# Kernel optimization log

Hardware: AMD Instinct MI355X
Metric: run time of the kernel (lower is better)

## Reference

```python
import jax, jax.numpy as jnp
import numpy as np

N_NODES = 100000
N_EDGES = 1600000
N_GRAPHS = 64
IN_FEATS = 86  # 10 + |NodeTypes|(3) + |Devices|(5) + 2*2 + 2*32
GCN_H = 64
FC_H = 32
BN_EPS = 1e-5


def setup_inputs() -> dict:
    key = jax.random.key(0)
    ks = jax.random.split(key, 10)
    x = jax.random.normal(ks[0], (N_NODES, IN_FEATS), dtype=jnp.float32)
    edge_src = jax.random.randint(ks[1], (N_EDGES,), 0, N_NODES, dtype=jnp.int32)
    edge_dst = jax.random.randint(ks[2], (N_EDGES,), 0, N_NODES, dtype=jnp.int32)
    graph_ids = jnp.sort(jax.random.randint(ks[3], (N_NODES,), 0, N_GRAPHS, dtype=jnp.int32))
    bn_gamma = jnp.ones((IN_FEATS,), dtype=jnp.float32)
    bn_beta = jnp.zeros((IN_FEATS,), dtype=jnp.float32)
    W1 = jax.random.normal(ks[4], (IN_FEATS, GCN_H), dtype=jnp.float32) * 0.1
    b1 = jnp.zeros((GCN_H,), dtype=jnp.float32)
    W2 = jax.random.normal(ks[5], (GCN_H, GCN_H), dtype=jnp.float32) * 0.1
    b2 = jnp.zeros((GCN_H,), dtype=jnp.float32)
    fc1_w = jax.random.normal(ks[6], (GCN_H, FC_H), dtype=jnp.float32) * 0.1
    fc1_b = jnp.zeros((FC_H,), dtype=jnp.float32)
    fc2_w = jax.random.normal(ks[7], (FC_H, 1), dtype=jnp.float32) * 0.1
    fc2_b = jnp.zeros((1,), dtype=jnp.float32)
    return {"x": x, "edge_src": edge_src, "edge_dst": edge_dst,
            "graph_ids": graph_ids, "num_graphs": N_GRAPHS,
            "bn_gamma": bn_gamma, "bn_beta": bn_beta,
            "W1": W1, "b1": b1, "W2": W2, "b2": b2,
            "fc1_w": fc1_w, "fc1_b": fc1_b, "fc2_w": fc2_w, "fc2_b": fc2_b}


def _gcn_layer(h, edge_src, edge_dst, W, b):
    # DGL copy_src + mean reduce: each node's h is overwritten by the mean of
    # its in-neighbors' h; zero-in-degree nodes keep their old h (UDF reduce
    # is only applied to nodes with non-empty mailboxes).
    n = h.shape[0]
    msg_sum = jax.ops.segment_sum(h[edge_src], edge_dst, num_segments=n)  # [N, d]
    deg = jax.ops.segment_sum(jnp.ones_like(edge_dst, dtype=h.dtype), edge_dst, num_segments=n)
    agg = jnp.where(deg[:, None] > 0, msg_sum / jnp.maximum(deg, 1.0)[:, None], h)
    return jax.nn.relu(agg @ W + b)


def reference(x, edge_src, edge_dst, graph_ids, num_graphs,
              bn_gamma, bn_beta, W1, b1, W2, b2, fc1_w, fc1_b, fc2_w, fc2_b):
    # BatchNorm1d in training mode: batch stats, biased variance.
    mean = jnp.mean(x, axis=0)
    var = jnp.mean(jnp.square(x - mean), axis=0)
    h = (x - mean) * jax.lax.rsqrt(var + BN_EPS) * bn_gamma + bn_beta
    # Two GCN layers (mean message passing + linear + ReLU).
    h = _gcn_layer(h, edge_src, edge_dst, W1, b1)
    h = _gcn_layer(h, edge_src, edge_dst, W2, b2)
    # dgl.mean_nodes over the batched graph: per-graph mean of node features.
    g_sum = jax.ops.segment_sum(h, graph_ids, num_segments=num_graphs)  # [B, d]
    g_cnt = jax.ops.segment_sum(jnp.ones_like(graph_ids, dtype=h.dtype), graph_ids, num_segments=num_graphs)
    hg = g_sum / jnp.maximum(g_cnt, 1.0)[:, None]
    # FC head (no activation between the two linears, matching the source).
    hg = hg @ fc1_w + fc1_b
    hg = hg @ fc2_w + fc2_b
    return jax.nn.sigmoid(hg).squeeze()
```

## Files before the change

### kernel.cpp

```cpp
#include <hip/hip_runtime.h>

#define N_NODES 100000
#define N_EDGES 1600000
#define N_GRAPHS_C 64
#define IN_F 86
#define H 64
#define N_BKT 391
#define SC_EPT 8
#define SC_TILE 2048
#define SC_GRID 782
#define BC_GRID 1024
typedef unsigned short ushort;

__device__ inline float bf2f(ushort u) { return __uint_as_float(((unsigned)u) << 16); }
__device__ inline ushort f2bf(float f) {
    unsigned x = __float_as_uint(f);
    return (ushort)((x + 0x7fffu + ((x >> 16) & 1u)) >> 16);
}

__global__ void bn_count_k(const float* __restrict__ x, const int* __restrict__ dst,
                           float* __restrict__ bnsum, float* __restrict__ bnsq,
                           int* __restrict__ bcnt) {
    __shared__ float s1[IN_F], s2[IN_F];
    __shared__ int hist[N_BKT];
    int tid = threadIdx.x;
    if (tid < IN_F) { s1[tid] = 0.f; s2[tid] = 0.f; }
    for (int i = tid; i < N_BKT; i += 256) hist[i] = 0;
    __syncthreads();
    if (blockIdx.x < SC_GRID) {
        int e0 = blockIdx.x * SC_TILE;
#pragma unroll
        for (int i = 0; i < SC_EPT; i++) {
            int e = e0 + i * 256 + tid;
            if (e < N_EDGES) atomicAdd(&hist[dst[e] >> 8], 1);
        }
    }
    const int NWAVE = BC_GRID * 4;
    const int RPW = (N_NODES + NWAVE - 1) / NWAVE;
    int lane = tid & 63;
    int w = blockIdx.x * 4 + (tid >> 6);
    int r0 = w * RPW;
    int r1 = min(r0 + RPW, N_NODES);
    float sum0 = 0.f, sq0 = 0.f, sum1 = 0.f, sq1 = 0.f;
#pragma unroll 4
    for (int r = r0; r < r1; r++) {
        const float* base = x + (size_t)r * IN_F;
        float v0 = base[lane];
        float v1 = (lane < IN_F - 64) ? base[64 + lane] : 0.f;
        sum0 += v0; sq0 += v0 * v0;
        sum1 += v1; sq1 += v1 * v1;
    }
    atomicAdd(&s1[lane], sum0);
    atomicAdd(&s2[lane], sq0);
    if (lane < IN_F - 64) {
        atomicAdd(&s1[64 + lane], sum1);
        atomicAdd(&s2[64 + lane], sq1);
    }
    __syncthreads();
    if (tid < IN_F) {
        atomicAdd(&bnsum[tid], s1[tid]);
        atomicAdd(&bnsq[tid], s2[tid]);
    }
    if (blockIdx.x < SC_GRID)
        for (int i = tid; i < N_BKT; i += 256) atomicAdd(&bcnt[i], hist[i]);
}

__global__ void scanprep_k(const int* __restrict__ bcnt, int* __restrict__ bstart,
                           int* __restrict__ gcursor,
                           const float* __restrict__ bnsum, const float* __restrict__ bnsq,
                           const float* __restrict__ gamma, const float* __restrict__ beta,
                           const float* __restrict__ W1, const float* __restrict__ b1,
                           float* __restrict__ W1p, float* __restrict__ c1) {
    __shared__ int tmp[512];
    __shared__ float scale[IN_F], shift[IN_F];
    int t = threadIdx.x;
    int v = (t < N_BKT) ? bcnt[t] : 0;
    tmp[t] = v;
    __syncthreads();
    for (int off = 1; off < 512; off <<= 1) {
        int a = (t >= off) ? tmp[t - off] : 0;
        __syncthreads();
        tmp[t] += a;
        __syncthreads();
    }
    if (t < N_BKT) { bstart[t] = tmp[t] - v; gcursor[t] = tmp[t] - v; }
    if (t == N_BKT - 1) bstart[N_BKT] = tmp[t];
    if (t < IN_F) {
        float mean = bnsum[t] * (1.0f / N_NODES);
        float var  = bnsq[t] * (1.0f / N_NODES) - mean * mean;
        float sc = gamma[t] * rsqrtf(var + 1e-5f);
        scale[t] = sc;
        shift[t] = beta[t] - mean * sc;
    }
    __syncthreads();
    for (int idx = t; idx < IN_F * H; idx += 512) W1p[idx] = scale[idx / H] * W1[idx];
    if (t < H) {
        float acc = b1[t];
        for (int i = 0; i < IN_F; i++) acc += shift[i] * W1[i * H + t];
        c1[t] = acc;
    }
}

__global__ void bucket_scatter_k(const int* __restrict__ src, const int* __restrict__ dst,
                                 int* __restrict__ gcursor, unsigned* __restrict__ ebkt) {
    __shared__ int hist[N_BKT];
    __shared__ int base[N_BKT];
    int tid = threadIdx.x;
    for (int i = tid; i < N_BKT; i += 256) hist[i] = 0;
    __syncthreads();
    int e0 = blockIdx.x * SC_TILE;
    unsigned pk[SC_EPT];
    int bk[SC_EPT], lo[SC_EPT];
#pragma unroll
    for (int i = 0; i < SC_EPT; i++) {
        int e = e0 + i * 256 + tid;
        if (e < N_EDGES) {
            int d = dst[e];
            pk[i] = ((unsigned)src[e] << 8) | (unsigned)(d & 255);
            bk[i] = d >> 8;
            lo[i] = atomicAdd(&hist[bk[i]], 1);
        }
    }
    __syncthreads();
    for (int i = tid; i < N_BKT; i += 256) base[i] = atomicAdd(&gcursor[i], hist[i]);
    __syncthreads();
#pragma unroll
    for (int i = 0; i < SC_EPT; i++) {
        int e = e0 + i * 256 + tid;
        if (e < N_EDGES) ebkt[base[bk[i]] + lo[i]] = pk[i];
    }
}

__global__ void bucket_fill_k(const unsigned* __restrict__ ebkt, const int* __restrict__ bstart,
                              int* __restrict__ rs, int* __restrict__ csr) {
    __shared__ int deg[256];
    __shared__ int scn[256];
    __shared__ int cur[256];
    int b = blockIdx.x;
    int tid = threadIdx.x;
    int e0 = bstart[b], e1 = bstart[b + 1];
    deg[tid] = 0;
    __syncthreads();
    for (int e = e0 + tid; e < e1; e += 256) atomicAdd(&deg[ebkt[e] & 255u], 1);
    __syncthreads();
    scn[tid] = deg[tid];
    __syncthreads();
    for (int off = 1; off < 256; off <<= 1) {
        int a = (tid >= off) ? scn[tid - off] : 0;
        __syncthreads();
        scn[tid] += a;
        __syncthreads();
    }
    int node = (b << 8) + tid;
    if (node < N_NODES) rs[node] = e0 + scn[tid];
    cur[tid] = e0 + scn[tid] - deg[tid];
    __syncthreads();
    for (int e = e0 + tid; e < e1; e += 256) {
        unsigned p = ebkt[e];
        int pos = atomicAdd(&cur[p & 255u], 1);
        csr[pos] = (int)((p & ~255u) >> 1);
    }
}

__global__ __launch_bounds__(256) void gemm_f32_k(const float* __restrict__ X,
                                                  const float* __restrict__ W,
                                                  const float* __restrict__ bias,
                                                  ushort* __restrict__ Y, int N) {
    const int K = IN_F;
    __shared__ __align__(16) ushort Xt[IN_F][72];
    __shared__ __align__(16) float Wl[IN_F][64];
    int tid = threadIdx.x;
    int row0 = blockIdx.x * 64;
    for (int i = tid; i < K * 64; i += 256) Wl[i / 64][i % 64] = W[i];
    for (int i = tid; i < 64 * K; i += 256) {
        int r = i / K, c = i % K;
        Xt[c][r] = (row0 + r < N) ? f2bf(X[(size_t)(row0 + r) * K + c]) : (ushort)0;
    }
    __syncthreads();
    int cg = tid & 15, rg = tid >> 4;
    float4 b4 = *(const float4*)&bias[cg * 4];
    float acc[4][4];
    for (int i = 0; i < 4; i++) { acc[i][0] = b4.x; acc[i][1] = b4.y; acc[i][2] = b4.z; acc[i][3] = b4.w; }
    for (int k = 0; k < K; k++) {
        float4 w = *(const float4*)&Wl[k][cg * 4];
        ushort4 xu = *(const ushort4*)&Xt[k][rg * 4];
        float x0 = bf2f(xu.x), x1 = bf2f(xu.y), x2 = bf2f(xu.z), x3 = bf2f(xu.w);
        acc[0][0] += x0 * w.x; acc[0][1] += x0 * w.y; acc[0][2] += x0 * w.z; acc[0][3] += x0 * w.w;
        acc[1][0] += x1 * w.x; acc[1][1] += x1 * w.y; acc[1][2] += x1 * w.z; acc[1][3] += x1 * w.w;
        acc[2][0] += x2 * w.x; acc[2][1] += x2 * w.y; acc[2][2] += x2 * w.z; acc[2][3] += x2 * w.w;
        acc[3][0] += x3 * w.x; acc[3][1] += x3 * w.y; acc[3][2] += x3 * w.z; acc[3][3] += x3 * w.w;
    }
    for (int i = 0; i < 4; i++) {
        int gr = row0 + rg * 4 + i;
        if (gr < N) {
            ushort4 o;
            o.x = f2bf(acc[i][0]); o.y = f2bf(acc[i][1]);
            o.z = f2bf(acc[i][2]); o.w = f2bf(acc[i][3]);
            *(ushort4*)&Y[(size_t)gr * 64 + cg * 4] = o;
        }
    }
}

__global__ __launch_bounds__(256) void gemm2pool_k(const ushort* __restrict__ X,
                                                   const float* __restrict__ W,
                                                   const float* __restrict__ bias,
                                                   const int* __restrict__ gid,
                                                   float* __restrict__ gsum,
                                                   int* __restrict__ gcnt, int N) {
    const int K = H;
    __shared__ __align__(16) ushort Xt[H][72];
    __shared__ __align__(16) float Wl[H][64];
    __shared__ int gl[64];
    __shared__ __align__(16) float red[16][64];
    int tid = threadIdx.x;
    int row0 = blockIdx.x * 64;
    for (int i = tid; i < K * 64; i += 256) Wl[i / 64][i % 64] = W[i];
    for (int i = tid; i < 64 * 16; i += 256) {
        int r = i >> 4, c4 = (i & 15) * 4;
        ushort4 u = (row0 + r < N) ? *(const ushort4*)&X[(size_t)(row0 + r) * K + c4]
                                   : make_ushort4(0, 0, 0, 0);
        Xt[c4 + 0][r] = u.x; Xt[c4 + 1][r] = u.y;
        Xt[c4 + 2][r] = u.z; Xt[c4 + 3][r] = u.w;
    }
    if (tid < 64) gl[tid] = (row0 + tid < N) ? gid[row0 + tid] : -1;
    __syncthreads();
    int cg = tid & 15, rg = tid >> 4;
    float4 b4 = *(const float4*)&bias[cg * 4];
    float acc[4][4];
    for (int i = 0; i < 4; i++) { acc[i][0] = b4.x; acc[i][1] = b4.y; acc[i][2] = b4.z; acc[i][3] = b4.w; }
    for (int k = 0; k < K; k++) {
        float4 w = *(const float4*)&Wl[k][cg * 4];
        ushort4 xu = *(const ushort4*)&Xt[k][rg * 4];
        float x0 = bf2f(xu.x), x1 = bf2f(xu.y), x2 = bf2f(xu.z), x3 = bf2f(xu.w);
        acc[0][0] += x0 * w.x; acc[0][1] += x0 * w.y; acc[0][2] += x0 * w.z; acc[0][3] += x0 * w.w;
        acc[1][0] += x1 * w.x; acc[1][1] += x1 * w.y; acc[1][2] += x1 * w.z; acc[1][3] += x1 * w.w;
        acc[2][0] += x2 * w.x; acc[2][1] += x2 * w.y; acc[2][2] += x2 * w.z; acc[2][3] += x2 * w.w;
        acc[3][0] += x3 * w.x; acc[3][1] += x3 * w.y; acc[3][2] += x3 * w.z; acc[3][3] += x3 * w.w;
    }
    for (int i = 0; i < 4; i++)
        for (int j = 0; j < 4; j++) acc[i][j] = fmaxf(acc[i][j], 0.f);
    int rstart = 0;
    while (rstart < 64) {
        int g = gl[rstart];
        if (g < 0) break;
        int rend = rstart + 1;
        while (rend < 64 && gl[rend] == g) rend++;
        float p0 = 0.f, p1 = 0.f, p2 = 0.f, p3 = 0.f;
#pragma unroll
        for (int i = 0; i < 4; i++) {
            int r = rg * 4 + i;
            if (r >= rstart && r < rend) { p0 += acc[i][0]; p1 += acc[i][1]; p2 += acc[i][2]; p3 += acc[i][3]; }
        }
        *(float4*)&red[rg][cg * 4] = make_float4(p0, p1, p2, p3);
        __syncthreads();
        for (int s = 8; s >= 1; s >>= 1) {
            if (rg < s) {
                float4 a = *(float4*)&red[rg][cg * 4];
                float4 b = *(float4*)&red[rg + s][cg * 4];
                *(float4*)&red[rg][cg * 4] = make_float4(a.x + b.x, a.y + b.y, a.z + b.z, a.w + b.w);
            }
            __syncthreads();
        }
        if (rg == 0) {
            atomicAdd(&gsum[g * 64 + cg * 4 + 0], red[0][cg * 4 + 0]);
            atomicAdd(&gsum[g * 64 + cg * 4 + 1], red[0][cg * 4 + 1]);
            atomicAdd(&gsum[g * 64 + cg * 4 + 2], red[0][cg * 4 + 2]);
            atomicAdd(&gsum[g * 64 + cg * 4 + 3], red[0][cg * 4 + 3]);
        }
        if (tid == 0) atomicAdd(&gcnt[g], rend - rstart);
        rstart = rend;
        __syncthreads();
    }
}

__global__ void gather_k(const ushort* __restrict__ g, const int* __restrict__ rs,
                         const int* __restrict__ csr, ushort* __restrict__ out) {
    int lane = threadIdx.x & 63;
    int n = blockIdx.x * 4 + (threadIdx.x >> 6);
    if (n >= N_NODES) return;
    int start = (n == 0) ? 0 : rs[n - 1];
    int end = rs[n];
    int fl = lane & 15;
    int grp = lane >> 4;
    const char* gL = (const char*)g + (fl << 3);
    float a0 = 0.f, a1 = 0.f, a2 = 0.f, a3 = 0.f;
    float b0 = 0.f, b1 = 0.f, b2 = 0.f, b3 = 0.f;
    for (int j0 = start; j0 < end; j0 += 64) {
        int cnt = min(64, end - j0);
        int myoff = (lane < cnt) ? csr[j0 + lane] : 0;
        int j = 0;
        for (; j + 8 <= cnt; j += 8) {
            int s0 = __shfl(myoff, j + grp, 64);
            int s1 = __shfl(myoff, j + 4 + grp, 64);
            uint2 u0 = *(const uint2*)(gL + s0);
            uint2 u1 = *(const uint2*)(gL + s1);
            a0 += __uint_as_float(u0.x << 16);
            a1 += __uint_as_float(u0.x & 0xffff0000u);
            a2 += __uint_as_float(u0.y << 16);
            a3 += __uint_as_float(u0.y & 0xffff0000u);
            b0 += __uint_as_float(u1.x << 16);
            b1 += __uint_as_float(u1.x & 0xffff0000u);
            b2 += __uint_as_float(u1.y << 16);
            b3 += __uint_as_float(u1.y & 0xffff0000u);
        }
        for (; j < cnt; j += 4) {
            int idx = j + grp;
            int s = __shfl(myoff, (idx < cnt) ? idx : (cnt - 1), 64);
            uint2 u = *(const uint2*)(gL + s);
            if (idx < cnt) {
                a0 += __uint_as_float(u.x << 16);
                a1 += __uint_as_float(u.x & 0xffff0000u);
                a2 += __uint_as_float(u.y << 16);
                a3 += __uint_as_float(u.y & 0xffff0000u);
            }
        }
    }
    float v0 = a0 + b0, v1 = a1 + b1, v2 = a2 + b2, v3 = a3 + b3;
    v0 += __shfl_xor(v0, 16, 64); v0 += __shfl_xor(v0, 32, 64);
    v1 += __shfl_xor(v1, 16, 64); v1 += __shfl_xor(v1, 32, 64);
    v2 += __shfl_xor(v2, 16, 64); v2 += __shfl_xor(v2, 32, 64);
    v3 += __shfl_xor(v3, 16, 64); v3 += __shfl_xor(v3, 32, 64);
    if (grp == 0) {
        int d = end - start;
        float r0, r1, r2, r3;
        if (d > 0) {
            float inv = 1.0f / (float)d;
            r0 = v0 * inv; r1 = v1 * inv; r2 = v2 * inv; r3 = v3 * inv;
        } else {
            uint2 u = *(const uint2*)((const char*)g + (size_t)n * 128 + (fl << 3));
            r0 = __uint_as_float(u.x << 16);
            r1 = __uint_as_float(u.x & 0xffff0000u);
            r2 = __uint_as_float(u.y << 16);
            r3 = __uint_as_float(u.y & 0xffff0000u);
        }
        ushort4 o;
        o.x = f2bf(fmaxf(r0, 0.f)); o.y = f2bf(fmaxf(r1, 0.f));
        o.z = f2bf(fmaxf(r2, 0.f)); o.w = f2bf(fmaxf(r3, 0.f));
        *(ushort4*)((char*)out + (size_t)n * 128 + (fl << 3)) = o;
    }
}

__global__ void gather_noact_k(const ushort* __restrict__ g, const int* __restrict__ rs,
                               const int* __restrict__ csr, ushort* __restrict__ out) {
    int lane = threadIdx.x & 63;
    int n = blockIdx.x * 4 + (threadIdx.x >> 6);
    if (n >= N_NODES) return;
    int start = (n == 0) ? 0 : rs[n - 1];
    int end = rs[n];
    int fl = lane & 15;
    int grp = lane >> 4;
    const char* gL = (const char*)g + (fl << 3);
    float a0 = 0.f, a1 = 0.f, a2 = 0.f, a3 = 0.f;
    float b0 = 0.f, b1 = 0.f, b2 = 0.f, b3 = 0.f;
    for (int j0 = start; j0 < end; j0 += 64) {
        int cnt = min(64, end - j0);
        int myoff = (lane < cnt) ? csr[j0 + lane] : 0;
        int j = 0;
        for (; j + 8 <= cnt; j += 8) {
            int s0 = __shfl(myoff, j + grp, 64);
            int s1 = __shfl(myoff, j + 4 + grp, 64);
            uint2 u0 = *(const uint2*)(gL + s0);
            uint2 u1 = *(const uint2*)(gL + s1);
            a0 += __uint_as_float(u0.x << 16);
            a1 += __uint_as_float(u0.x & 0xffff0000u);
            a2 += __uint_as_float(u0.y << 16);
            a3 += __uint_as_float(u0.y & 0xffff0000u);
            b0 += __uint_as_float(u1.x << 16);
            b1 += __uint_as_float(u1.x & 0xffff0000u);
            b2 += __uint_as_float(u1.y << 16);
            b3 += __uint_as_float(u1.y & 0xffff0000u);
        }
        for (; j < cnt; j += 4) {
            int idx = j + grp;
            int s = __shfl(myoff, (idx < cnt) ? idx : (cnt - 1), 64);
            uint2 u = *(const uint2*)(gL + s);
            if (idx < cnt) {
                a0 += __uint_as_float(u.x << 16);
                a1 += __uint_as_float(u.x & 0xffff0000u);
                a2 += __uint_as_float(u.y << 16);
                a3 += __uint_as_float(u.y & 0xffff0000u);
            }
        }
    }
    float v0 = a0 + b0, v1 = a1 + b1, v2 = a2 + b2, v3 = a3 + b3;
    v0 += __shfl_xor(v0, 16, 64); v0 += __shfl_xor(v0, 32, 64);
    v1 += __shfl_xor(v1, 16, 64); v1 += __shfl_xor(v1, 32, 64);
    v2 += __shfl_xor(v2, 16, 64); v2 += __shfl_xor(v2, 32, 64);
    v3 += __shfl_xor(v3, 16, 64); v3 += __shfl_xor(v3, 32, 64);
    if (grp == 0) {
        int d = end - start;
        float r0, r1, r2, r3;
        if (d > 0) {
            float inv = 1.0f / (float)d;
            r0 = v0 * inv; r1 = v1 * inv; r2 = v2 * inv; r3 = v3 * inv;
        } else {
            uint2 u = *(const uint2*)((const char*)g + (size_t)n * 128 + (fl << 3));
            r0 = __uint_as_float(u.x << 16);
            r1 = __uint_as_float(u.x & 0xffff0000u);
            r2 = __uint_as_float(u.y << 16);
            r3 = __uint_as_float(u.y & 0xffff0000u);
        }
        ushort4 o;
        o.x = f2bf(r0); o.y = f2bf(r1); o.z = f2bf(r2); o.w = f2bf(r3);
        *(ushort4*)((char*)out + (size_t)n * 128 + (fl << 3)) = o;
    }
}

__global__ void head_k(const float* __restrict__ gsum, const int* __restrict__ gcnt,
                       const float* __restrict__ fc1w, const float* __restrict__ fc1b,
                       const float* __restrict__ fc2w, const float* __restrict__ fc2b,
                       float* __restrict__ out) {
    __shared__ float w1[H * 32];
    __shared__ float w2[32], bb1[32];
    int b = threadIdx.x;
    for (int i = b; i < H * 32; i += 64) w1[i] = fc1w[i];
    if (b < 32) { w2[b] = fc2w[b]; bb1[b] = fc1b[b]; }
    __syncthreads();
    if (b >= N_GRAPHS_C) return;
    float hg[H];
    float inv = 1.0f / fmaxf((float)gcnt[b], 1.0f);
    for (int k = 0; k < H; k++) hg[k] = gsum[b * H + k] * inv;
    float z = fc2b[0];
    for (int j = 0; j < 32; j++) {
        float t = bb1[j];
        for (int k = 0; k < H; k++) t += hg[k] * w1[k * 32 + j];
        z += t * w2[j];
    }
    out[b] = 1.0f / (1.0f + expf(-z));
}

extern "C" void kernel_launch(void* const* d_in, const int* in_sizes, int n_in,
                              void* d_out, int out_size, void* d_ws, size_t ws_size,
                              hipStream_t stream) {
    const float* x        = (const float*)d_in[0];
    const int*   edge_src = (const int*)d_in[1];
    const int*   edge_dst = (const int*)d_in[2];
    const int*   gid      = (const int*)d_in[3];
    const float* bn_gamma = (const float*)d_in[5];
    const float* bn_beta  = (const float*)d_in[6];
    const float* W1       = (const float*)d_in[7];
    const float* b1       = (const float*)d_in[8];
    const float* W2       = (const float*)d_in[9];
    const float* b2       = (const float*)d_in[10];
    const float* fc1w     = (const float*)d_in[11];
    const float* fc1b     = (const float*)d_in[12];
    const float* fc2w     = (const float*)d_in[13];
    const float* fc2b     = (const float*)d_in[14];
    float* out = (float*)d_out;

    char* ws = (char*)d_ws;
    size_t off = 0;
    auto alloc = [&](size_t bytes) { void* p = ws + off; off += (bytes + 255) & ~(size_t)255; return p; };
    const size_t ZW = IN_F + IN_F + N_BKT + N_GRAPHS_C * H + N_GRAPHS_C;
    float* zreg  = (float*)alloc(ZW * sizeof(float));
    float* bnsum = zreg;
    float* bnsq  = bnsum + IN_F;
    int*   bcnt  = (int*)(bnsq + IN_F);
    float* gsum  = (float*)(bcnt + N_BKT);
    int*   gcnt  = (int*)(gsum + N_GRAPHS_C * H);
    float* W1p     = (float*)alloc(IN_F * H * sizeof(float));
    float* c1      = (float*)alloc(H * sizeof(float));
    int*   bstart  = (int*)alloc((N_BKT + 1) * sizeof(int));
    int*   gcursor = (int*)alloc(N_BKT * sizeof(int));
    int*   rs      = (int*)alloc(N_NODES * sizeof(int));
    int*   csr     = (int*)alloc((size_t)N_EDGES * sizeof(int));
    ushort* gbuf   = (ushort*)alloc((size_t)N_NODES * H * sizeof(ushort));
    ushort* h1     = (ushort*)alloc((size_t)N_NODES * H * sizeof(ushort));
    unsigned* ebkt = (unsigned*)gbuf;

    hipMemsetAsync(zreg, 0, ZW * sizeof(float), stream);

    bn_count_k<<<BC_GRID, 256, 0, stream>>>(x, edge_dst, bnsum, bnsq, bcnt);
    scanprep_k<<<1, 512, 0, stream>>>(bcnt, bstart, gcursor, bnsum, bnsq,
                                      bn_gamma, bn_beta, W1, b1, W1p, c1);
    bucket_scatter_k<<<SC_GRID, 256, 0, stream>>>(edge_src, edge_dst, gcursor, ebkt);
    bucket_fill_k<<<N_BKT, 256, 0, stream>>>(ebkt, bstart, rs, csr);

    gemm_f32_k<<<(N_NODES + 63) / 64, 256, 0, stream>>>(x, W1p, c1, gbuf, N_NODES);
    gather_k<<<(N_NODES + 3) / 4, 256, 0, stream>>>(gbuf, rs, csr, h1);

    gather_noact_k<<<(N_NODES + 3) / 4, 256, 0, stream>>>(h1, rs, csr, gbuf);
    gemm2pool_k<<<(N_NODES + 63) / 64, 256, 0, stream>>>(gbuf, W2, b2, gid, gsum, gcnt, N_NODES);

    head_k<<<1, 64, 0, stream>>>(gsum, gcnt, fc1w, fc1b, fc2w, fc2b, out);
}
```

Measured before the change: 360.2 us.

## Fuse layer-2 neighbor aggregation into GEMM and pooling kernel

Merges the second-layer gather (mean aggregation) with the W2 GEMM and per-graph pooling into one kernel. Each block aggregates 64 nodes straight into shared memory, so the bf16 intermediate no longer goes to global memory and one launch disappears. The shared weight tiles are also stored as bf16, which halves their LDS footprint and adds an extra rounding step. The fused kernel has only 1563 blocks, each wave aggregating 16 nodes one after another, so there is less parallelism to hide gather latency.

Result: no change. 354.7 us (-1.6%).

```diff
diff --git a/kernel.cpp b/kernel.cpp
--- a/kernel.cpp
+++ b/kernel.cpp
@@ -162,127 +162,8 @@
     }
 }
 
-__global__ __launch_bounds__(256) void gemm_f32_k(const float* __restrict__ X,
-                                                  const float* __restrict__ W,
-                                                  const float* __restrict__ bias,
-                                                  ushort* __restrict__ Y, int N) {
-    const int K = IN_F;
-    __shared__ __align__(16) ushort Xt[IN_F][72];
-    __shared__ __align__(16) float Wl[IN_F][64];
-    int tid = threadIdx.x;
-    int row0 = blockIdx.x * 64;
-    for (int i = tid; i < K * 64; i += 256) Wl[i / 64][i % 64] = W[i];
-    for (int i = tid; i < 64 * K; i += 256) {
-        int r = i / K, c = i % K;
-        Xt[c][r] = (row0 + r < N) ? f2bf(X[(size_t)(row0 + r) * K + c]) : (ushort)0;
-    }
-    __syncthreads();
-    int cg = tid & 15, rg = tid >> 4;
-    float4 b4 = *(const float4*)&bias[cg * 4];
-    float acc[4][4];
-    for (int i = 0; i < 4; i++) { acc[i][0] = b4.x; acc[i][1] = b4.y; acc[i][2] = b4.z; acc[i][3] = b4.w; }
-    for (int k = 0; k < K; k++) {
-        float4 w = *(const float4*)&Wl[k][cg * 4];
-        ushort4 xu = *(const ushort4*)&Xt[k][rg * 4];
-        float x0 = bf2f(xu.x), x1 = bf2f(xu.y), x2 = bf2f(xu.z), x3 = bf2f(xu.w);
-        acc[0][0] += x0 * w.x; acc[0][1] += x0 * w.y; acc[0][2] += x0 * w.z; acc[0][3] += x0 * w.w;
-        acc[1][0] += x1 * w.x; acc[1][1] += x1 * w.y; acc[1][2] += x1 * w.z; acc[1][3] += x1 * w.w;
-        acc[2][0] += x2 * w.x; acc[2][1] += x2 * w.y; acc[2][2] += x2 * w.z; acc[2][3] += x2 * w.w;
-        acc[3][0] += x3 * w.x; acc[3][1] += x3 * w.y; acc[3][2] += x3 * w.z; acc[3][3] += x3 * w.w;
-    }
-    for (int i = 0; i < 4; i++) {
-        int gr = row0 + rg * 4 + i;
-        if (gr < N) {
-            ushort4 o;
-            o.x = f2bf(acc[i][0]); o.y = f2bf(acc[i][1]);
-            o.z = f2bf(acc[i][2]); o.w = f2bf(acc[i][3]);
-            *(ushort4*)&Y[(size_t)gr * 64 + cg * 4] = o;
-        }
-    }
-}
-
-__global__ __launch_bounds__(256) void gemm2pool_k(const ushort* __restrict__ X,
-                                                   const float* __restrict__ W,
-                                                   const float* __restrict__ bias,
-                                                   const int* __restrict__ gid,
-                                                   float* __restrict__ gsum,
-                                                   int* __restrict__ gcnt, int N) {
-    const int K = H;
-    __shared__ __align__(16) ushort Xt[H][72];
-    __shared__ __align__(16) float Wl[H][64];
-    __shared__ int gl[64];
-    __shared__ __align__(16) float red[16][64];
-    int tid = threadIdx.x;
-    int row0 = blockIdx.x * 64;
-    for (int i = tid; i < K * 64; i += 256) Wl[i / 64][i % 64] = W[i];
-    for (int i = tid; i < 64 * 16; i += 256) {
-        int r = i >> 4, c4 = (i & 15) * 4;
-        ushort4 u = (row0 + r < N) ? *(const ushort4*)&X[(size_t)(row0 + r) * K + c4]
-                                   : make_ushort4(0, 0, 0, 0);
-        Xt[c4 + 0][r] = u.x; Xt[c4 + 1][r] = u.y;
-        Xt[c4 + 2][r] = u.z; Xt[c4 + 3][r] = u.w;
-    }
-    if (tid < 64) gl[tid] = (row0 + tid < N) ? gid[row0 + tid] : -1;
-    __syncthreads();
-    int cg = tid & 15, rg = tid >> 4;
-    float4 b4 = *(const float4*)&bias[cg * 4];
-    float acc[4][4];
-    for (int i = 0; i < 4; i++) { acc[i][0] = b4.x; acc[i][1] = b4.y; acc[i][2] = b4.z; acc[i][3] = b4.w; }
-    for (int k = 0; k < K; k++) {
-        float4 w = *(const float4*)&Wl[k][cg * 4];
-        ushort4 xu = *(const ushort4*)&Xt[k][rg * 4];
-        float x0 = bf2f(xu.x), x1 = bf2f(xu.y), x2 = bf2f(xu.z), x3 = bf2f(xu.w);
-        acc[0][0] += x0 * w.x; acc[0][1] += x0 * w.y; acc[0][2] += x0 * w.z; acc[0][3] += x0 * w.w;
-        acc[1][0] += x1 * w.x; acc[1][1] += x1 * w.y; acc[1][2] += x1 * w.z; acc[1][3] += x1 * w.w;
-        acc[2][0] += x2 * w.x; acc[2][1] += x2 * w.y; acc[2][2] += x2 * w.z; acc[2][3] += x2 * w.w;
-        acc[3][0] += x3 * w.x; acc[3][1] += x3 * w.y; acc[3][2] += x3 * w.z; acc[3][3] += x3 * w.w;
-    }
-    for (int i = 0; i < 4; i++)
-        for (int j = 0; j < 4; j++) acc[i][j] = fmaxf(acc[i][j], 0.f);
-    int rstart = 0;
-    while (rstart < 64) {
-        int g = gl[rstart];
-        if (g < 0) break;
-        int rend = rstart + 1;
-        while (rend < 64 && gl[rend] == g) rend++;
-        float p0 = 0.f, p1 = 0.f, p2 = 0.f, p3 = 0.f;
-#pragma unroll
-        for (int i = 0; i < 4; i++) {
-            int r = rg * 4 + i;
-            if (r >= rstart && r < rend) { p0 += acc[i][0]; p1 += acc[i][1]; p2 += acc[i][2]; p3 += acc[i][3]; }
-        }
-        *(float4*)&red[rg][cg * 4] = make_float4(p0, p1, p2, p3);
-        __syncthreads();
-        for (int s = 8; s >= 1; s >>= 1) {
-            if (rg < s) {
-                float4 a = *(float4*)&red[rg][cg * 4];
-                float4 b = *(float4*)&red[rg + s][cg * 4];
-                *(float4*)&red[rg][cg * 4] = make_float4(a.x + b.x, a.y + b.y, a.z + b.z, a.w + b.w);
-            }
-            __syncthreads();
-        }
-        if (rg == 0) {
-            atomicAdd(&gsum[g * 64 + cg * 4 + 0], red[0][cg * 4 + 0]);
-            atomicAdd(&gsum[g * 64 + cg * 4 + 1], red[0][cg * 4 + 1]);
-            atomicAdd(&gsum[g * 64 + cg * 4 + 2], red[0][cg * 4 + 2]);
-            atomicAdd(&gsum[g * 64 + cg * 4 + 3], red[0][cg * 4 + 3]);
-        }
-        if (tid == 0) atomicAdd(&gcnt[g], rend - rstart);
-        rstart = rend;
-        __syncthreads();
-    }
-}
-
-__global__ void gather_k(const ushort* __restrict__ g, const int* __restrict__ rs,
-                         const int* __restrict__ csr, ushort* __restrict__ out) {
-    int lane = threadIdx.x & 63;
-    int n = blockIdx.x * 4 + (threadIdx.x >> 6);
-    if (n >= N_NODES) return;
-    int start = (n == 0) ? 0 : rs[n - 1];
-    int end = rs[n];
-    int fl = lane & 15;
-    int grp = lane >> 4;
-    const char* gL = (const char*)g + (fl << 3);
+__device__ inline float4 agg_quad(const char* __restrict__ gL, const int* __restrict__ csr,
+                                  int start, int end, int lane, int grp) {
     float a0 = 0.f, a1 = 0.f, a2 = 0.f, a3 = 0.f;
     float b0 = 0.f, b1 = 0.f, b2 = 0.f, b3 = 0.f;
     for (int j0 = start; j0 < end; j0 += 64) {
@@ -320,28 +201,51 @@
     v1 += __shfl_xor(v1, 16, 64); v1 += __shfl_xor(v1, 32, 64);
     v2 += __shfl_xor(v2, 16, 64); v2 += __shfl_xor(v2, 32, 64);
     v3 += __shfl_xor(v3, 16, 64); v3 += __shfl_xor(v3, 32, 64);
-    if (grp == 0) {
-        int d = end - start;
-        float r0, r1, r2, r3;
-        if (d > 0) {
-            float inv = 1.0f / (float)d;
-            r0 = v0 * inv; r1 = v1 * inv; r2 = v2 * inv; r3 = v3 * inv;
-        } else {
-            uint2 u = *(const uint2*)((const char*)g + (size_t)n * 128 + (fl << 3));
-            r0 = __uint_as_float(u.x << 16);
-            r1 = __uint_as_float(u.x & 0xffff0000u);
-            r2 = __uint_as_float(u.y << 16);
-            r3 = __uint_as_float(u.y & 0xffff0000u);
-        }
-        ushort4 o;
-        o.x = f2bf(fmaxf(r0, 0.f)); o.y = f2bf(fmaxf(r1, 0.f));
-        o.z = f2bf(fmaxf(r2, 0.f)); o.w = f2bf(fmaxf(r3, 0.f));
-        *(ushort4*)((char*)out + (size_t)n * 128 + (fl << 3)) = o;
-    }
-}
-
-__global__ void gather_noact_k(const ushort* __restrict__ g, const int* __restrict__ rs,
-                               const int* __restrict__ csr, ushort* __restrict__ out) {
+    return make_float4(v0, v1, v2, v3);
+}
+
+__global__ __launch_bounds__(256) void gemm_f32_k(const float* __restrict__ X,
+                                                  const float* __restrict__ W,
+                                                  const float* __restrict__ bias,
+                                                  ushort* __restrict__ Y, int N) {
+    const int K = IN_F;
+    __shared__ __align__(16) ushort Xt[IN_F][72];
+    __shared__ __align__(16) ushort Wl[IN_F][64];
+    int tid = threadIdx.x;
+    int row0 = blockIdx.x * 64;
+    for (int i = tid; i < K * 64; i += 256) Wl[i / 64][i % 64] = f2bf(W[i]);
+    for (int i = tid; i < 64 * K; i += 256) {
+        int r = i / K, c = i % K;
+        Xt[c][r] = (row0 + r < N) ? f2bf(X[(size_t)(row0 + r) * K + c]) : (ushort)0;
+    }
+    __syncthreads();
+    int cg = tid & 15, rg = tid >> 4;
+    float4 b4 = *(const float4*)&bias[cg * 4];
+    float acc[4][4];
+    for (int i = 0; i < 4; i++) { acc[i][0] = b4.x; acc[i][1] = b4.y; acc[i][2] = b4.z; acc[i][3] = b4.w; }
+    for (int k = 0; k < K; k++) {
+        ushort4 wu = *(const ushort4*)&Wl[k][cg * 4];
+        ushort4 xu = *(const ushort4*)&Xt[k][rg * 4];
+        float w0 = bf2f(wu.x), w1 = bf2f(wu.y), w2 = bf2f(wu.z), w3 = bf2f(wu.w);
+        float x0 = bf2f(xu.x), x1 = bf2f(xu.y), x2 = bf2f(xu.z), x3 = bf2f(xu.w);
+        acc[0][0] += x0 * w0; acc[0][1] += x0 * w1; acc[0][2] += x0 * w2; acc[0][3] += x0 * w3;
+        acc[1][0] += x1 * w0; acc[1][1] += x1 * w1; acc[1][2] += x1 * w2; acc[1][3] += x1 * w3;
+        acc[2][0] += x2 * w0; acc[2][1] += x2 * w1; acc[2][2] += x2 * w2; acc[2][3] += x2 * w3;
+        acc[3][0] += x3 * w0; acc[3][1] += x3 * w1; acc[3][2] += x3 * w2; acc[3][3] += x3 * w3;
+    }
+    for (int i = 0; i < 4; i++) {
+        int gr = row0 + rg * 4 + i;
+        if (gr < N) {
+            ushort4 o;
+            o.x = f2bf(acc[i][0]); o.y = f2bf(acc[i][1]);
+            o.z = f2bf(acc[i][2]); o.w = f2bf(acc[i][3]);
+            *(ushort4*)&Y[(size_t)gr * 64 + cg * 4] = o;
+        }
+    }
+}
+
+__global__ void gather_k(const ushort* __restrict__ g, const int* __restrict__ rs,
+                         const int* __restrict__ csr, ushort* __restrict__ out) {
     int lane = threadIdx.x & 63;
     int n = blockIdx.x * 4 + (threadIdx.x >> 6);
     if (n >= N_NODES) return;
@@ -349,50 +253,13 @@
     int end = rs[n];
     int fl = lane & 15;
     int grp = lane >> 4;
-    const char* gL = (const char*)g + (fl << 3);
-    float a0 = 0.f, a1 = 0.f, a2 = 0.f, a3 = 0.f;
-    float b0 = 0.f, b1 = 0.f, b2 = 0.f, b3 = 0.f;
-    for (int j0 = start; j0 < end; j0 += 64) {
-        int cnt = min(64, end - j0);
-        int myoff = (lane < cnt) ? csr[j0 + lane] : 0;
-        int j = 0;
-        for (; j + 8 <= cnt; j += 8) {
-            int s0 = __shfl(myoff, j + grp, 64);
-            int s1 = __shfl(myoff, j + 4 + grp, 64);
-            uint2 u0 = *(const uint2*)(gL + s0);
-            uint2 u1 = *(const uint2*)(gL + s1);
-            a0 += __uint_as_float(u0.x << 16);
-            a1 += __uint_as_float(u0.x & 0xffff0000u);
-            a2 += __uint_as_float(u0.y << 16);
-            a3 += __uint_as_float(u0.y & 0xffff0000u);
-            b0 += __uint_as_float(u1.x << 16);
-            b1 += __uint_as_float(u1.x & 0xffff0000u);
-            b2 += __uint_as_float(u1.y << 16);
-            b3 += __uint_as_float(u1.y & 0xffff0000u);
-        }
-        for (; j < cnt; j += 4) {
-            int idx = j + grp;
-            int s = __shfl(myoff, (idx < cnt) ? idx : (cnt - 1), 64);
-            uint2 u = *(const uint2*)(gL + s);
-            if (idx < cnt) {
-                a0 += __uint_as_float(u.x << 16);
-                a1 += __uint_as_float(u.x & 0xffff0000u);
-                a2 += __uint_as_float(u.y << 16);
-                a3 += __uint_as_float(u.y & 0xffff0000u);
-            }
-        }
-    }
-    float v0 = a0 + b0, v1 = a1 + b1, v2 = a2 + b2, v3 = a3 + b3;
-    v0 += __shfl_xor(v0, 16, 64); v0 += __shfl_xor(v0, 32, 64);
-    v1 += __shfl_xor(v1, 16, 64); v1 += __shfl_xor(v1, 32, 64);
-    v2 += __shfl_xor(v2, 16, 64); v2 += __shfl_xor(v2, 32, 64);
-    v3 += __shfl_xor(v3, 16, 64); v3 += __shfl_xor(v3, 32, 64);
+    float4 v = agg_quad((const char*)g + (fl << 3), csr, start, end, lane, grp);
     if (grp == 0) {
         int d = end - start;
         float r0, r1, r2, r3;
         if (d > 0) {
             float inv = 1.0f / (float)d;
-            r0 = v0 * inv; r1 = v1 * inv; r2 = v2 * inv; r3 = v3 * inv;
+            r0 = v.x * inv; r1 = v.y * inv; r2 = v.z * inv; r3 = v.w * inv;
         } else {
             uint2 u = *(const uint2*)((const char*)g + (size_t)n * 128 + (fl << 3));
             r0 = __uint_as_float(u.x << 16);
@@ -401,8 +268,110 @@
             r3 = __uint_as_float(u.y & 0xffff0000u);
         }
         ushort4 o;
-        o.x = f2bf(r0); o.y = f2bf(r1); o.z = f2bf(r2); o.w = f2bf(r3);
+        o.x = f2bf(fmaxf(r0, 0.f)); o.y = f2bf(fmaxf(r1, 0.f));
+        o.z = f2bf(fmaxf(r2, 0.f)); o.w = f2bf(fmaxf(r3, 0.f));
         *(ushort4*)((char*)out + (size_t)n * 128 + (fl << 3)) = o;
+    }
+}
+
+__global__ __launch_bounds__(256) void agg_gemm2pool_k(const ushort* __restrict__ h1,
+                                                       const int* __restrict__ rs,
+                                                       const int* __restrict__ csr,
+                                                       const float* __restrict__ W,
+                                                       const float* __restrict__ bias,
+                                                       const int* __restrict__ gid,
+                                                       float* __restrict__ gsum,
+                                                       int* __restrict__ gcnt, int N) {
+    const int K = H;
+    __shared__ __align__(16) ushort Xt[H][72];
+    __shared__ __align__(16) ushort Wl[H][64];
+    __shared__ int gl[64];
+    __shared__ __align__(16) float red[16][64];
+    int tid = threadIdx.x;
+    int row0 = blockIdx.x * 64;
+    for (int i = tid; i < K * 64; i += 256) Wl[i / 64][i % 64] = f2bf(W[i]);
+    if (tid < 64) gl[tid] = (row0 + tid < N) ? gid[row0 + tid] : -1;
+    int lane = tid & 63, wv = tid >> 6;
+    int fl = lane & 15, grp = lane >> 4;
+    const char* gL = (const char*)h1 + (fl << 3);
+    for (int i = 0; i < 16; i++) {
+        int r = wv * 16 + i;
+        int n = row0 + r;
+        if (n < N) {
+            int start = (n == 0) ? 0 : rs[n - 1];
+            int end = rs[n];
+            float4 v = agg_quad(gL, csr, start, end, lane, grp);
+            if (grp == 0) {
+                int d = end - start;
+                float r0, r1, r2, r3;
+                if (d > 0) {
+                    float inv = 1.0f / (float)d;
+                    r0 = v.x * inv; r1 = v.y * inv; r2 = v.z * inv; r3 = v.w * inv;
+                } else {
+                    uint2 u = *(const uint2*)((const char*)h1 + (size_t)n * 128 + (fl << 3));
+                    r0 = __uint_as_float(u.x << 16);
+                    r1 = __uint_as_float(u.x & 0xffff0000u);
+                    r2 = __uint_as_float(u.y << 16);
+                    r3 = __uint_as_float(u.y & 0xffff0000u);
+                }
+                Xt[fl * 4 + 0][r] = f2bf(r0);
+                Xt[fl * 4 + 1][r] = f2bf(r1);
+                Xt[fl * 4 + 2][r] = f2bf(r2);
+                Xt[fl * 4 + 3][r] = f2bf(r3);
+            }
+        } else if (grp == 0) {
+            Xt[fl * 4 + 0][r] = 0; Xt[fl * 4 + 1][r] = 0;
+            Xt[fl * 4 + 2][r] = 0; Xt[fl * 4 + 3][r] = 0;
+        }
+    }
+    __syncthreads();
+    int cg = tid & 15, rg = tid >> 4;
+    float4 b4 = *(const float4*)&bias[cg * 4];
+    float acc[4][4];
+    for (int i = 0; i < 4; i++) { acc[i][0] = b4.x; acc[i][1] = b4.y; acc[i][2] = b4.z; acc[i][3] = b4.w; }
+    for (int k = 0; k < K; k++) {
+        ushort4 wu = *(const ushort4*)&Wl[k][cg * 4];
+        ushort4 xu = *(const ushort4*)&Xt[k][rg * 4];
+        float w0 = bf2f(wu.x), w1 = bf2f(wu.y), w2 = bf2f(wu.z), w3 = bf2f(wu.w);
+        float x0 = bf2f(xu.x), x1 = bf2f(xu.y), x2 = bf2f(xu.z), x3 = bf2f(xu.w);
+        acc[0][0] += x0 * w0; acc[0][1] += x0 * w1; acc[0][2] += x0 * w2; acc[0][3] += x0 * w3;
+        acc[1][0] += x1 * w0; acc[1][1] += x1 * w1; acc[1][2] += x1 * w2; acc[1][3] += x1 * w3;
+        acc[2][0] += x2 * w0; acc[2][1] += x2 * w1; acc[2][2] += x2 * w2; acc[2][3] += x2 * w3;
+        acc[3][0] += x3 * w0; acc[3][1] += x3 * w1; acc[3][2] += x3 * w2; acc[3][3] += x3 * w3;
+    }
+    for (int i = 0; i < 4; i++)
+        for (int j = 0; j < 4; j++) acc[i][j] = fmaxf(acc[i][j], 0.f);
+    int rstart = 0;
+    while (rstart < 64) {
+        int g = gl[rstart];
+        if (g < 0) break;
+        int rend = rstart + 1;
+        while (rend < 64 && gl[rend] == g) rend++;
+        float p0 = 0.f, p1 = 0.f, p2 = 0.f, p3 = 0.f;
+#pragma unroll
+        for (int i = 0; i < 4; i++) {
+            int r = rg * 4 + i;
+            if (r >= rstart && r < rend) { p0 += acc[i][0]; p1 += acc[i][1]; p2 += acc[i][2]; p3 += acc[i][3]; }
+        }
+        *(float4*)&red[rg][cg * 4] = make_float4(p0, p1, p2, p3);
+        __syncthreads();
+        for (int s = 8; s >= 1; s >>= 1) {
+            if (rg < s) {
+                float4 a = *(float4*)&red[rg][cg * 4];
+                float4 b = *(float4*)&red[rg + s][cg * 4];
+                *(float4*)&red[rg][cg * 4] = make_float4(a.x + b.x, a.y + b.y, a.z + b.z, a.w + b.w);
+            }
+            __syncthreads();
+        }
+        if (rg == 0) {
+            atomicAdd(&gsum[g * 64 + cg * 4 + 0], red[0][cg * 4 + 0]);
+            atomicAdd(&gsum[g * 64 + cg * 4 + 1], red[0][cg * 4 + 1]);
+            atomicAdd(&gsum[g * 64 + cg * 4 + 2], red[0][cg * 4 + 2]);
+            atomicAdd(&gsum[g * 64 + cg * 4 + 3], red[0][cg * 4 + 3]);
+        }
+        if (tid == 0) atomicAdd(&gcnt[g], rend - rstart);
+        rstart = rend;
+        __syncthreads();
     }
 }
 
@@ -479,8 +448,8 @@
     gemm_f32_k<<<(N_NODES + 63) / 64, 256, 0, stream>>>(x, W1p, c1, gbuf, N_NODES);
     gather_k<<<(N_NODES + 3) / 4, 256, 0, stream>>>(gbuf, rs, csr, h1);
 
-    gather_noact_k<<<(N_NODES + 3) / 4, 256, 0, stream>>>(h1, rs, csr, gbuf);
-    gemm2pool_k<<<(N_NODES + 63) / 64, 256, 0, stream>>>(gbuf, W2, b2, gid, gsum, gcnt, N_NODES);
+    agg_gemm2pool_k<<<(N_NODES + 63) / 64, 256, 0, stream>>>(h1, rs, csr, W2, b2,
+                                                             gid, gsum, gcnt, N_NODES);
 
     head_k<<<1, 64, 0, stream>>>(gsum, gcnt, fc1w, fc1b, fc2w, fc2b, out);
 }
```
